# Kernel tuning notes

Hardware: AMD Instinct MI355X
Metric: run time of the kernel (lower is better)

Reference implementation:

```python
import jax, jax.numpy as jnp
import numpy as np
from jax import lax

KERNEL = 3
CIN = 512
FMAPS = 512
LATENT = 512
GAIN = 1.0
LRMUL = 1.0
# StyleGAN2 wscale: runtime_coef = gain / sqrt(fan_in) * lrmul
RC_W = GAIN / np.sqrt(KERNEL * KERNEL * CIN) * LRMUL
RC_S = GAIN / np.sqrt(LATENT) * LRMUL


def setup_inputs() -> dict:
    key = jax.random.key(0)
    k1, k2, k3, k4, k5 = jax.random.split(key, 5)
    N, H, W = 8, 64, 64
    x = jax.random.normal(k1, (N, CIN, H, W), dtype=jnp.float32)
    dlatent_vect = jax.random.normal(k2, (N, LATENT), dtype=jnp.float32)
    weight = jax.random.normal(k3, (KERNEL, KERNEL, CIN, FMAPS), dtype=jnp.float32)
    mod_weight = jax.random.normal(k4, (LATENT, CIN), dtype=jnp.float32)
    mod_bias = jax.random.normal(k5, (CIN,), dtype=jnp.float32)
    return {"x": x, "dlatent_vect": dlatent_vect, "weight": weight,
            "mod_weight": mod_weight, "mod_bias": mod_bias}


def reference(x, dlatent_vect, weight, mod_weight, mod_bias):
    N, _, H, W = x.shape
    w = weight * RC_W                                       # [kh,kw,Cin,Cout]
    # style: s = A(dlatent) + 1
    s = dlatent_vect @ (mod_weight * RC_S) + mod_bias * LRMUL + 1.0  # [N,Cin]
    # per-sample modulated weights
    ww = w[None] * s[:, None, None, :, None]                # [N,kh,kw,Cin,Cout]
    # demodulate
    d = lax.rsqrt(jnp.sum(jnp.square(ww), axis=(1, 2, 3)) + 1e-8)  # [N,Cout]
    ww = ww * d[:, None, None, None, :]
    # fused modconv: one grouped conv with N groups
    xr = x.reshape(1, N * CIN, H, W)
    wr = jnp.transpose(ww, (1, 2, 3, 0, 4)).reshape(KERNEL, KERNEL, CIN, N * FMAPS)
    out = lax.conv_general_dilated(
        xr, wr, window_strides=(1, 1), padding="SAME",
        dimension_numbers=("NCHW", "HWIO", "NCHW"),
        feature_group_count=N)
    return out.reshape(N, FMAPS, H, W)
```

## Files before the change

kernel.cpp:

```cpp
#include <hip/hip_runtime.h>
#include <math.h>

#define CIN_    512
#define COUT_   512
#define LATENT_ 512
#define NB_     8
#define HH_     64
#define WW_     64

typedef float f32x16 __attribute__((ext_vector_type(16)));
typedef short bf16x8v __attribute__((ext_vector_type(8)));

__device__ inline unsigned short f2bf(float f) {
    union { float f; unsigned u; } v; v.f = f;
    unsigned r = v.u + 0x7fffu + ((v.u >> 16) & 1u);
    return (unsigned short)(r >> 16);
}

__device__ __forceinline__ void gl_lds16(const void* g, void* l) {
    __builtin_amdgcn_global_load_lds(
        (const __attribute__((address_space(1))) unsigned int*)g,
        (__attribute__((address_space(3))) unsigned int*)l,
        16, 0, 0);
}

__global__ __launch_bounds__(256) void prep1(
    const float* __restrict__ w, const float* __restrict__ dlat,
    const float* __restrict__ mw, const float* __restrict__ mb,
    float* __restrict__ wsq, unsigned short* __restrict__ wb,
    float* __restrict__ s)
{
    __shared__ float smem[16 * 521];
    const float RC_W = 0.0147313912747197f;
    const float RC_S = 0.0441941738241592f;
    int b = blockIdx.x;
    int t = threadIdx.x;

    if (b < 1024) {
        int idx = b * 256 + t;
        float acc = 0.f;
#pragma unroll
        for (int tap = 0; tap < 9; ++tap) {
            float v = w[tap * (CIN_ * COUT_) + idx];
            acc += v * v;
        }
        wsq[idx] = acc;
    } else if (b < 1312) {
        int bb  = b - 1024;
        int tap = bb / 32;
        int cb  = bb % 32;
        for (int idx = t; idx < 16 * 512; idx += 256) {
            int ci = idx >> 9;
            int co = idx & 511;
            smem[ci * 521 + co] = w[((size_t)tap * 512 + cb * 16 + ci) * 512 + co];
        }
        __syncthreads();
        unsigned short* dst = wb + (size_t)(tap * 32 + cb) * 512 * 16;
        for (int idx = t; idx < 16 * 512; idx += 256) {
            int co = idx >> 4;
            int ci = idx & 15;
            dst[idx] = f2bf(smem[ci * 521 + co] * RC_W);
        }
    } else {
        int bb  = b - 1312;
        int n   = bb >> 3;
        int ci0 = (bb & 7) * 64;
        for (int i = t; i < LATENT_; i += 256) smem[i] = dlat[n * LATENT_ + i];
        __syncthreads();
        int cil  = t & 63;
        int part = t >> 6;
        const float* mwp = mw + ci0 + cil;
        float a0 = 0.f, a1 = 0.f;
        int l0 = part * 128;
#pragma unroll 4
        for (int l = l0; l < l0 + 128; l += 2) {
            a0 += smem[l]     * mwp[(size_t)l * CIN_];
            a1 += smem[l + 1] * mwp[(size_t)(l + 1) * CIN_];
        }
        smem[512 + part * 64 + cil] = a0 + a1;
        __syncthreads();
        if (t < 64) {
            float r = smem[512 + t] + smem[576 + t] + smem[640 + t] + smem[704 + t];
            s[n * CIN_ + ci0 + t] = r * RC_S + mb[ci0 + t] + 1.0f;
        }
    }
}

__global__ __launch_bounds__(256) void prep2(
    const float* __restrict__ x, const float* __restrict__ s,
    const float* __restrict__ wsq, float* __restrict__ dmod,
    unsigned short* __restrict__ xt)
{
    __shared__ float smem[16 * 67 + 16];
    int b = blockIdx.x;
    int t = threadIdx.x;

    if (b < 64) {
        const float RCW2 = 1.0f / 4608.0f;
        int n   = b >> 3;
        int co0 = (b & 7) * 64;
        for (int i = t; i < CIN_; i += 256) { float v = s[n * CIN_ + i]; smem[i] = v * v; }
        __syncthreads();
        int col  = t & 63;
        int part = t >> 6;
        const float* wp = wsq + co0 + col;
        float a0 = 0.f, a1 = 0.f;
        int c0 = part * 128;
#pragma unroll 4
        for (int ci = c0; ci < c0 + 128; ci += 2) {
            a0 += smem[ci]     * wp[(size_t)ci * COUT_];
            a1 += smem[ci + 1] * wp[(size_t)(ci + 1) * COUT_];
        }
        smem[512 + part * 64 + col] = a0 + a1;
        __syncthreads();
        if (t < 64) {
            float r = smem[512 + t] + smem[576 + t] + smem[640 + t] + smem[704 + t];
            dmod[n * COUT_ + co0 + t] = rsqrtf(RCW2 * r + 1e-8f);
        }
    } else {
        int bb = b - 64;
        int hp = bb % 66;
        int cb = (bb / 66) % 32;
        int n  = bb / (66 * 32);
        int gh = hp - 1;
        bool rowok = (gh >= 0) && (gh < HH_);

        if (t < 16) smem[16 * 67 + t] = s[n * CIN_ + cb * 16 + t];
        if (rowok) {
            const float* src = &x[(((size_t)n * CIN_ + cb * 16) * HH_ + gh) * WW_];
            int ci = t >> 4;
            int g0 = (t & 15) * 4;
            float4 v = *(const float4*)&src[(size_t)ci * (HH_ * WW_) + g0];
            float* dstl = &smem[ci * 67 + g0];
            dstl[0] = v.x; dstl[1] = v.y; dstl[2] = v.z; dstl[3] = v.w;
        }
        __syncthreads();

        unsigned short* dst = xt + (((size_t)(n * 32 + cb) * 66 + hp) * 66) * 16;
        for (int p = t; p < 264; p += 256) {
            int e   = p * 4;
            int wp_ = e >> 4;
            int cie = e & 15;
            int gw  = wp_ - 1;
            float vv0 = 0.f, vv1 = 0.f, vv2 = 0.f, vv3 = 0.f;
            if (rowok && gw >= 0 && gw < WW_) {
                vv0 = smem[(cie + 0) * 67 + gw] * smem[16 * 67 + cie + 0];
                vv1 = smem[(cie + 1) * 67 + gw] * smem[16 * 67 + cie + 1];
                vv2 = smem[(cie + 2) * 67 + gw] * smem[16 * 67 + cie + 2];
                vv3 = smem[(cie + 3) * 67 + gw] * smem[16 * 67 + cie + 3];
            }
            ushort4 o4;
            o4.x = f2bf(vv0); o4.y = f2bf(vv1); o4.z = f2bf(vv2); o4.w = f2bf(vv3);
            *(ushort4*)&dst[e] = o4;
        }
    }
}

__global__ __launch_bounds__(256) void conv_mfma(
    const unsigned short* __restrict__ xt,
    const unsigned short* __restrict__ wb,
    const float* __restrict__ dmod,
    float* __restrict__ out)
{
    __shared__ __align__(16) union {
        struct { unsigned short xs[2880]; unsigned short ws[18432]; } s;
        float o[64 * 129];
    } sm;

    int b   = blockIdx.x;
    int cot = b & 3;
    int wt_ = (b >> 2) & 3;
    int ht  = (b >> 4) & 7;
    int n   = b >> 7;
    int h0 = ht * 8, w0 = wt_ * 16, co0 = cot * 128;

    int t    = threadIdx.x;
    int wv   = t >> 6, lane = t & 63;
    int mh   = wv >> 1, nh = wv & 1;
    int l5   = lane & 31, half = lane >> 5;

    f32x16 acc[2][2];
#pragma unroll
    for (int ms = 0; ms < 2; ++ms)
#pragma unroll
        for (int ns = 0; ns < 2; ++ns)
#pragma unroll
            for (int i = 0; i < 16; ++i) acc[ms][ns][i] = 0.f;

    for (int cb = 0; cb < 32; ++cb) {
        const unsigned short* xb = xt + (((size_t)(n * 32 + cb) * 66 + h0) * 66 + w0) * 16;
        for (int li = t; li < 360; li += 256) {
            int row = li / 36;
            int off = li - row * 36;
            gl_lds16(&xb[row * 1056 + off * 8], &sm.s.xs[(li - lane) * 8]);
        }
        const unsigned short* wbb = wb + ((size_t)cb * 512 + co0) * 16;
#pragma unroll
        for (int tap = 0; tap < 9; ++tap) {
            gl_lds16(&wbb[(size_t)tap * 32 * 512 * 16 + t * 8],
                     &sm.s.ws[tap * 2048 + wv * 512]);
        }
        __syncthreads();

#pragma unroll
        for (int tap = 0; tap < 9; ++tap) {
            int kh = tap / 3, kw = tap - 3 * (tap / 3);
            bf16x8v bfr[2], afr[2];
#pragma unroll
            for (int ns = 0; ns < 2; ++ns) {
                int co_l = nh * 64 + ns * 32 + l5;
                bfr[ns] = *(const bf16x8v*)&sm.s.ws[tap * 2048 + co_l * 16 + half * 8];
            }
#pragma unroll
            for (int ms = 0; ms < 2; ++ms) {
                int pr = mh * 4 + ms * 2 + (l5 >> 4);
                int pc = l5 & 15;
                int pos = (pr + kh) * 18 + (pc + kw);
                afr[ms] = *(const bf16x8v*)&sm.s.xs[pos * 16 + half * 8];
            }
#pragma unroll
            for (int ms = 0; ms < 2; ++ms)
#pragma unroll
                for (int ns = 0; ns < 2; ++ns)
                    acc[ms][ns] = __builtin_amdgcn_mfma_f32_32x32x16_bf16(
                        afr[ms], bfr[ns], acc[ms][ns], 0, 0, 0);
        }
        __syncthreads();
    }

    for (int p = 0; p < 2; ++p) {
        __syncthreads();
        int co_l = nh * 64 + p * 32 + l5;
        int bco  = nh * 32 + l5;
        float dv = dmod[n * COUT_ + co0 + co_l];
#pragma unroll
        for (int ms = 0; ms < 2; ++ms) {
#pragma unroll
            for (int reg = 0; reg < 16; ++reg) {
                int ml = (reg & 3) + 8 * (reg >> 2) + 4 * half;
                int pr = mh * 4 + ms * 2 + (ml >> 4);
                int pc = ml & 15;
                sm.o[bco * 129 + pr * 16 + pc] = acc[ms][p][reg] * dv;
            }
        }
        __syncthreads();
        for (int j = t; j < 2048; j += 256) {
            int wq = j & 3;
            int pairidx = j >> 2;
            int row  = pairidx & 7;
            int bco2 = pairidx >> 3;
            int co = (bco2 >> 5) * 64 + p * 32 + (bco2 & 31);
            const float* src = &sm.o[bco2 * 129 + row * 16 + wq * 4];
            float4 v = make_float4(src[0], src[1], src[2], src[3]);
            *(float4*)&out[(((size_t)n * COUT_ + co0 + co) * HH_ + h0 + row) * WW_ + w0 + wq * 4] = v;
        }
    }
}

extern "C" void kernel_launch(void* const* d_in, const int* in_sizes, int n_in,
                              void* d_out, int out_size, void* d_ws, size_t ws_size,
                              hipStream_t stream) {
    const float* x    = (const float*)d_in[0];
    const float* dlat = (const float*)d_in[1];
    const float* w    = (const float*)d_in[2];
    const float* mw   = (const float*)d_in[3];
    const float* mb   = (const float*)d_in[4];
    float* out = (float*)d_out;

    char* ws = (char*)d_ws;
    float* s    = (float*)(ws);
    float* dmod = (float*)(ws + 16384);
    float* wsq  = (float*)(ws + 32768);
    unsigned short* xt = (unsigned short*)(ws + 1081344);
    unsigned short* wb = (unsigned short*)(ws + 36765696);

    prep1<<<1376, 256, 0, stream>>>(w, dlat, mw, mb, wsq, wb, s);
    prep2<<<64 + NB_ * 32 * 66, 256, 0, stream>>>(x, s, wsq, dmod, xt);
    conv_mfma<<<1024, 256, 0, stream>>>(xt, wb, dmod, out);
}
```

Measured before the change: 292.4 us.

## Widen conv block tile to 256 output channels to reuse activation tiles

Each conv block now computes 256 output channels instead of 128, doubling the per-wave accumulator count and halving the grid to 512 blocks. Every activation tile loaded into LDS now feeds twice as many MFMAs, which cuts redundant input loads. The cost is twice the LDS for weights, higher register pressure (launch bounds set to 2 blocks), and fewer blocks than the 256 CUs can comfortably balance. The epilogue is reorganized so that half of the waves write each 64-channel slice.

```diff
diff --git a/kernel.cpp b/kernel.cpp
--- a/kernel.cpp
+++ b/kernel.cpp
@@ -156,60 +156,63 @@
     }
 }
 
-__global__ __launch_bounds__(256) void conv_mfma(
+__global__ __launch_bounds__(256, 2) void conv_mfma(
     const unsigned short* __restrict__ xt,
     const unsigned short* __restrict__ wb,
     const float* __restrict__ dmod,
     float* __restrict__ out)
 {
     __shared__ __align__(16) union {
-        struct { unsigned short xs[2880]; unsigned short ws[18432]; } s;
+        struct { unsigned short xs[2880]; unsigned short ws[36864]; } s;
         float o[64 * 129];
     } sm;
 
     int b   = blockIdx.x;
-    int cot = b & 3;
-    int wt_ = (b >> 2) & 3;
-    int ht  = (b >> 4) & 7;
-    int n   = b >> 7;
-    int h0 = ht * 8, w0 = wt_ * 16, co0 = cot * 128;
+    int cot = b & 1;
+    int wt_ = (b >> 1) & 3;
+    int ht  = (b >> 3) & 7;
+    int n   = b >> 6;
+    int h0 = ht * 8, w0 = wt_ * 16, co0 = cot * 256;
 
     int t    = threadIdx.x;
     int wv   = t >> 6, lane = t & 63;
     int mh   = wv >> 1, nh = wv & 1;
     int l5   = lane & 31, half = lane >> 5;
 
-    f32x16 acc[2][2];
+    f32x16 acc[2][4];
 #pragma unroll
     for (int ms = 0; ms < 2; ++ms)
 #pragma unroll
-        for (int ns = 0; ns < 2; ++ns)
+        for (int ns = 0; ns < 4; ++ns)
 #pragma unroll
             for (int i = 0; i < 16; ++i) acc[ms][ns][i] = 0.f;
 
     for (int cb = 0; cb < 32; ++cb) {
         const unsigned short* xb = xt + (((size_t)(n * 32 + cb) * 66 + h0) * 66 + w0) * 16;
-        for (int li = t; li < 360; li += 256) {
-            int row = li / 36;
-            int off = li - row * 36;
-            gl_lds16(&xb[row * 1056 + off * 8], &sm.s.xs[(li - lane) * 8]);
+        {
+            int li = t;
+            gl_lds16(&xb[(li / 36) * 1056 + (li % 36) * 8], &sm.s.xs[(li - lane) * 8]);
+            li = t + 256;
+            if (li < 360)
+                gl_lds16(&xb[(li / 36) * 1056 + (li % 36) * 8], &sm.s.xs[(li - lane) * 8]);
         }
         const unsigned short* wbb = wb + ((size_t)cb * 512 + co0) * 16;
 #pragma unroll
         for (int tap = 0; tap < 9; ++tap) {
-            gl_lds16(&wbb[(size_t)tap * 32 * 512 * 16 + t * 8],
-                     &sm.s.ws[tap * 2048 + wv * 512]);
+            const unsigned short* tsrc = wbb + (size_t)tap * 32 * 512 * 16;
+            gl_lds16(&tsrc[t * 8],         &sm.s.ws[tap * 4096 + wv * 512]);
+            gl_lds16(&tsrc[(t + 256) * 8], &sm.s.ws[tap * 4096 + 2048 + wv * 512]);
         }
         __syncthreads();
 
 #pragma unroll
         for (int tap = 0; tap < 9; ++tap) {
             int kh = tap / 3, kw = tap - 3 * (tap / 3);
-            bf16x8v bfr[2], afr[2];
-#pragma unroll
-            for (int ns = 0; ns < 2; ++ns) {
-                int co_l = nh * 64 + ns * 32 + l5;
-                bfr[ns] = *(const bf16x8v*)&sm.s.ws[tap * 2048 + co_l * 16 + half * 8];
+            bf16x8v bfr[4], afr[2];
+#pragma unroll
+            for (int ns = 0; ns < 4; ++ns) {
+                int co_l = nh * 128 + ns * 32 + l5;
+                bfr[ns] = *(const bf16x8v*)&sm.s.ws[tap * 4096 + co_l * 16 + half * 8];
             }
 #pragma unroll
             for (int ms = 0; ms < 2; ++ms) {
@@ -221,26 +224,29 @@
 #pragma unroll
             for (int ms = 0; ms < 2; ++ms)
 #pragma unroll
-                for (int ns = 0; ns < 2; ++ns)
+                for (int ns = 0; ns < 4; ++ns)
                     acc[ms][ns] = __builtin_amdgcn_mfma_f32_32x32x16_bf16(
                         afr[ms], bfr[ns], acc[ms][ns], 0, 0, 0);
         }
         __syncthreads();
     }
 
-    for (int p = 0; p < 2; ++p) {
-        __syncthreads();
-        int co_l = nh * 64 + p * 32 + l5;
-        int bco  = nh * 32 + l5;
-        float dv = dmod[n * COUT_ + co0 + co_l];
-#pragma unroll
-        for (int ms = 0; ms < 2; ++ms) {
-#pragma unroll
-            for (int reg = 0; reg < 16; ++reg) {
-                int ml = (reg & 3) + 8 * (reg >> 2) + 4 * half;
-                int pr = mh * 4 + ms * 2 + (ml >> 4);
-                int pc = ml & 15;
-                sm.o[bco * 129 + pr * 16 + pc] = acc[ms][p][reg] * dv;
+    for (int p = 0; p < 4; ++p) {
+        __syncthreads();
+        if (nh == (p >> 1)) {
+#pragma unroll
+            for (int q = 0; q < 2; ++q) {
+                int bco = q * 32 + l5;
+                float dv = dmod[n * COUT_ + co0 + p * 64 + bco];
+#pragma unroll
+                for (int ms = 0; ms < 2; ++ms) {
+#pragma unroll
+                    for (int reg = 0; reg < 16; ++reg) {
+                        int ml = (reg & 3) + 8 * (reg >> 2) + 4 * half;
+                        int m  = mh * 64 + ms * 32 + ml;
+                        sm.o[bco * 129 + m] = acc[ms][(p & 1) * 2 + q][reg] * dv;
+                    }
+                }
             }
         }
         __syncthreads();
@@ -249,10 +255,10 @@
             int pairidx = j >> 2;
             int row  = pairidx & 7;
             int bco2 = pairidx >> 3;
-            int co = (bco2 >> 5) * 64 + p * 32 + (bco2 & 31);
+            int co = co0 + p * 64 + bco2;
             const float* src = &sm.o[bco2 * 129 + row * 16 + wq * 4];
             float4 v = make_float4(src[0], src[1], src[2], src[3]);
-            *(float4*)&out[(((size_t)n * COUT_ + co0 + co) * HH_ + h0 + row) * WW_ + w0 + wq * 4] = v;
+            *(float4*)&out[(((size_t)n * COUT_ + co) * HH_ + h0 + row) * WW_ + w0 + wq * 4] = v;
         }
     }
 }
@@ -276,5 +282,5 @@
 
     prep1<<<1376, 256, 0, stream>>>(w, dlat, mw, mb, wsq, wb, s);
     prep2<<<64 + NB_ * 32 * 66, 256, 0, stream>>>(x, s, wsq, dmod, xt);
-    conv_mfma<<<1024, 256, 0, stream>>>(xt, wb, dmod, out);
-}
+    conv_mfma<<<512, 256, 0, stream>>>(xt, wb, dmod, out);
+}
```

After: 262.5 us. -10.2%, faster.
